# Kernel optimization log

Hardware: AMD Instinct MI355X
Metric: run time of the kernel (lower is better)

Reference implementation:

```python
import jax, jax.numpy as jnp
import numpy as np

B, D, V, S = 256, 784, 128, 2  # batch, dim, max_val, n_steps
ITER_PER_CYCLE = 10
STEP_SIZES = [0.5] + [0.1] * (ITER_PER_CYCLE - 1)   # sbc: [big_step] + [small_step]*...
BAL_CONSTS = [0.9] + [0.6] * (ITER_PER_CYCLE - 1)   # sbc: [big_bal] + [small_bal]*...
TEMP = 1.0


def setup_inputs() -> dict:
    key = jax.random.key(0)
    k1, k2, k3, k4, k5 = jax.random.split(key, 5)
    x = jax.random.randint(k1, (B, D), 0, V, dtype=jnp.int32)
    W = jax.random.normal(k2, (D, D), dtype=jnp.float32) * (1.0 / D)  # keep energies moderate
    b = jax.random.normal(k3, (D,), dtype=jnp.float32) * 0.1
    # Pre-sampled Gumbel noise for the categorical proposal (one slab per inner step)
    ug = jax.random.uniform(k4, (S, B, D, V), dtype=jnp.float32, minval=1e-6, maxval=1.0 - 1e-6)
    gumbel = -jnp.log(-jnp.log(ug))
    # Uniform draws for the MH accept/reject test
    u = jax.random.uniform(k5, (S, B), dtype=jnp.float32)
    k_iter = 0
    return {"x": x, "W": W, "b": b, "gumbel": gumbel, "u": u, "k_iter": k_iter}


def reference(x, W, b, gumbel, u, k_iter):
    step_size = STEP_SIZES[k_iter % ITER_PER_CYCLE]
    bal = BAL_CONSTS[k_iter % ITER_PER_CYCLE]
    Wsym = 0.5 * (W + W.T)

    def model(xf):                      # energy: [B]
        return 0.5 * jnp.einsum('bi,bi->b', xf, xf @ Wsym) + xf @ b

    def gradf(xf):                      # d(energy)/dx: [B, D]
        return xf @ Wsym + b

    disc = jnp.arange(V, dtype=jnp.float32)[None, None, :]  # [1,1,V]

    def calc_logits(xf, g):
        # term1 - term2 from _calc_logits, fused elementwise over [B, D, V]
        diff = disc - xf[:, :, None]
        return g[:, :, None] * diff * bal - diff * diff * (0.5 / step_size)

    def body(x_cur, inp):
        g_noise, ui = inp
        xf = x_cur.astype(jnp.float32)
        g = gradf(xf)
        logits = calc_logits(xf, g)                                  # [B,D,V]
        x_delta = jnp.argmax(logits + g_noise, axis=-1)              # categorical sample [B,D]
        logp = jax.nn.log_softmax(logits, axis=-1)
        lp_forward = jnp.take_along_axis(logp, x_delta[:, :, None], axis=-1)[..., 0].sum(axis=1)
        xdf = x_delta.astype(jnp.float32)
        gd = gradf(xdf) / TEMP
        logits_d = calc_logits(xdf, gd)
        logp_d = jax.nn.log_softmax(logits_d, axis=-1)
        lp_reverse = jnp.take_along_axis(logp_d, x_cur[:, :, None], axis=-1)[..., 0].sum(axis=1)
        la = model(xdf) - model(xf) + lp_reverse - lp_forward        # log accept ratio [B]
        acc = jnp.exp(la) > ui
        x_new = jnp.where(acc[:, None], x_delta, x_cur).astype(x_cur.dtype)
        return x_new, la

    x_out, las = jax.lax.scan(body, x, (gumbel, u))
    return x_out, las[-1]
```

## Files before the change

### kernel.cpp

```cpp
#include <hip/hip_runtime.h>

#define B_ 256
#define D_ 784
#define V_ 128
#define S_ 2
#define BD (B_ * D_)
#define KSPLIT 8
#define KC 98

__device__ __forceinline__ void get_params(const int* kiter, float& ss, float& bal) {
    int k = kiter[0] % 10;
    ss  = (k == 0) ? 0.5f : 0.1f;
    bal = (k == 0) ? 0.9f : 0.6f;
}

__device__ __forceinline__ double wave_red(double v) {
#pragma unroll
    for (int o = 32; o > 0; o >>= 1) v += __shfl_down(v, o, 64);
    return v;
}

__global__ __launch_bounds__(256) void symmetrize_k(
    const float* __restrict__ W, float* __restrict__ Wsym)
{
    __shared__ float tile[32][33];
    const int bx = blockIdx.x * 32, by = blockIdx.y * 32;
    const int tx = threadIdx.x & 31, ty4 = (threadIdx.x >> 5) * 4;
#pragma unroll
    for (int i = 0; i < 4; ++i) {
        int r = by + ty4 + i, c = bx + tx;
        tile[ty4 + i][tx] = (r < D_ && c < D_) ? W[r * D_ + c] : 0.f;
    }
    __syncthreads();
#pragma unroll
    for (int i = 0; i < 4; ++i) {
        int r = bx + ty4 + i, c = by + tx;
        if (r < D_ && c < D_)
            Wsym[r * D_ + c] = 0.5f * (W[r * D_ + c] + tile[tx][ty4 + i]);
    }
}

__global__ __launch_bounds__(256) void gemm_splitk(
    const int* __restrict__ Aint, const float* __restrict__ Wsym,
    float* __restrict__ Cp)
{
    const int bt = blockIdx.x, dt = blockIdx.y, kz = blockIdx.z;
    const int tid = threadIdx.x;
    const int k0 = kz * KC, kend = k0 + KC;

    __shared__ float As[64][20];
    __shared__ float Ws[16][68];

    const int tx = tid & 15, ty = tid >> 4;
    const int arow = tid >> 2, ac0 = (tid & 3) * 4;
    const int wrow = tid >> 4, wc0 = (tid & 15) * 4;
    const int wd0 = dt * 64 + wc0;

    float acc[4][4] = {};

    for (int kb = k0; kb < kend; kb += 16) {
#pragma unroll
        for (int c = 0; c < 4; ++c) {
            int k = kb + ac0 + c;
            As[arow][ac0 + c] = (k < kend) ? (float)Aint[(bt * 64 + arow) * D_ + k] : 0.f;
        }
        {
            int k = kb + wrow;
            float4 wv = (k < kend && wd0 < D_)
                ? *(const float4*)&Wsym[k * D_ + wd0]
                : make_float4(0.f, 0.f, 0.f, 0.f);
            *(float4*)&Ws[wrow][wc0] = wv;
        }
        __syncthreads();
#pragma unroll
        for (int kk = 0; kk < 16; kk += 4) {
            float va[4][4], vw[4][4];
#pragma unroll
            for (int i = 0; i < 4; ++i) {
                float4 t = *(const float4*)&As[ty * 4 + i][kk];
                va[i][0] = t.x; va[i][1] = t.y; va[i][2] = t.z; va[i][3] = t.w;
            }
#pragma unroll
            for (int m = 0; m < 4; ++m) {
                float4 t = *(const float4*)&Ws[kk + m][tx * 4];
                vw[m][0] = t.x; vw[m][1] = t.y; vw[m][2] = t.z; vw[m][3] = t.w;
            }
#pragma unroll
            for (int m = 0; m < 4; ++m)
#pragma unroll
                for (int i = 0; i < 4; ++i)
#pragma unroll
                    for (int j = 0; j < 4; ++j)
                        acc[i][j] = fmaf(va[i][m], vw[m][j], acc[i][j]);
        }
        __syncthreads();
    }

    const int d0 = dt * 64 + tx * 4;
    if (d0 < D_) {
#pragma unroll
        for (int i = 0; i < 4; ++i) {
            int bb = bt * 64 + ty * 4 + i;
            *(float4*)&Cp[(size_t)kz * BD + (size_t)bb * D_ + d0] =
                make_float4(acc[i][0], acc[i][1], acc[i][2], acc[i][3]);
        }
    }
}

__global__ __launch_bounds__(832) void forward_k(
    const int* __restrict__ xin, const float* __restrict__ gpart,
    const float* __restrict__ bvec, const float* __restrict__ gumbel,
    const int* __restrict__ kiter, int s,
    int* __restrict__ x_delta, double* __restrict__ lpf, double* __restrict__ Exf)
{
    const int b = blockIdx.x, tid = threadIdx.x;
    float ss, bal; get_params(kiter, ss, bal);
    const float c2 = 0.5f / ss;

    double lp_acc = 0.0, e_acc = 0.0;

    if (tid < D_) {
        const int d = tid, bd = b * D_ + d;
        const int xi = xin[bd];
        const float xfv = (float)xi;

        float gv = 0.f;
#pragma unroll
        for (int p = 0; p < KSPLIT; ++p) gv += gpart[(size_t)p * BD + bd];
        gv += bvec[d];

        const float a1 = bal * gv;
        const float v0 = xfv + a1 * ss;
        int vm = (int)rintf(v0); vm = min(127, max(0, vm));
        const float dmv = v0 - (float)vm;
        const float Reff = sqrtf(30.0f / c2 + dmv * dmv);
        int lo = max(0, (int)ceilf(v0 - Reff));
        int hi = min(127, (int)floorf(v0 + Reff));
        lo = min(lo, vm); hi = max(hi, vm);

        const float dvm = (float)vm - xfv;
        const float mL = dvm * fmaf(-c2, dvm, a1);

        const float4* __restrict__ gq =
            (const float4*)(gumbel + (((size_t)s * B_ + b) * D_ + d) * V_);
        const int q0 = lo >> 2, qh = hi >> 2;
        float4 quad[4];
#pragma unroll
        for (int j = 0; j < 4; ++j) quad[j] = gq[min(q0 + j, qh)];

        float best = -1e30f; int imax = vm;
        float sum0 = 0.f, sum1 = 0.f;
#pragma unroll
        for (int j = 0; j < 4; ++j) {
            const int qi = q0 + j;
            const bool qok = qi <= qh;
            const float qs[4] = {quad[j].x, quad[j].y, quad[j].z, quad[j].w};
#pragma unroll
            for (int c = 0; c < 4; ++c) {
                int v = 4 * qi + c;
                bool ok = qok && v >= lo && v <= hi;
                float dv = (float)v - xfv;
                float lg = dv * fmaf(-c2, dv, a1);
                float y = ok ? (lg + qs[c]) : -1e30f;
                if (y > best) { best = y; imax = v; }
                float e = expf(lg - mL);
                if (c & 1) sum1 += ok ? e : 0.f; else sum0 += ok ? e : 0.f;
            }
        }
        float lse = mL + logf(sum0 + sum1);
        float dvc = (float)imax - xfv;
        float lch = dvc * fmaf(-c2, dvc, a1);
        lp_acc = (double)(lch - lse);
        e_acc  = (double)xfv * ((double)gv + (double)bvec[d]);
        x_delta[bd] = imax;
    }

    __shared__ double wred[13];
    const int lane = tid & 63, wv = tid >> 6;
    double t = wave_red(lp_acc);
    if (lane == 0) wred[wv] = t;
    __syncthreads();
    if (tid == 0) { double sm = 0; for (int i = 0; i < 13; ++i) sm += wred[i]; lpf[b] = sm; }
    __syncthreads();
    t = wave_red(e_acc);
    if (lane == 0) wred[wv] = t;
    __syncthreads();
    if (tid == 0) { double sm = 0; for (int i = 0; i < 13; ++i) sm += wred[i]; Exf[b] = sm; }
}

__global__ __launch_bounds__(832) void reverse_k(
    const int* __restrict__ xin, int* __restrict__ x_cur,
    const int* __restrict__ x_delta,
    const float* __restrict__ gpart, const float* __restrict__ bvec,
    const float* __restrict__ u, const int* __restrict__ kiter,
    int s, int last, const double* __restrict__ lpf, const double* __restrict__ Exf,
    float* __restrict__ out)
{
    const int b = blockIdx.x, tid = threadIdx.x;
    float ss, bal; get_params(kiter, ss, bal);
    const float c2 = 0.5f / ss;

    double lp_acc = 0.0, e_acc = 0.0;

    if (tid < D_) {
        const int d = tid, bd = b * D_ + d;
        const int xi = xin[bd];
        const int xd = x_delta[bd];
        const float xdv = (float)xd;

        float gv = 0.f;
#pragma unroll
        for (int p = 0; p < KSPLIT; ++p) gv += gpart[(size_t)p * BD + bd];
        gv += bvec[d];

        const float a1 = bal * gv;
        const float v0 = xdv + a1 * ss;
        int vm = (int)rintf(v0); vm = min(127, max(0, vm));
        const float dmv = v0 - (float)vm;
        const float Reff = sqrtf(30.0f / c2 + dmv * dmv);
        int lo = max(0, (int)ceilf(v0 - Reff));
        int hi = min(127, (int)floorf(v0 + Reff));
        lo = min(lo, vm); hi = max(hi, vm);

        const float dvm = (float)vm - xdv;
        const float mL = dvm * fmaf(-c2, dvm, a1);
        float sum0 = 0.f, sum1 = 0.f;
#pragma unroll
        for (int j = 0; j < 16; ++j) {
            int v = lo + j;
            bool ok = v <= hi;
            float dv = (float)v - xdv;
            float lg = dv * fmaf(-c2, dv, a1);
            float e = expf(lg - mL);
            if (j & 1) sum1 += ok ? e : 0.f; else sum0 += ok ? e : 0.f;
        }
        float lse = mL + logf(sum0 + sum1);
        float dvc = (float)xi - xdv;
        float lch = dvc * fmaf(-c2, dvc, a1);
        lp_acc = (double)(lch - lse);
        e_acc  = (double)xdv * ((double)gv + (double)bvec[d]);
    }

    __shared__ double wred[13];
    __shared__ int accept_s;
    __shared__ float la_s;
    const int lane = tid & 63, wv = tid >> 6;

    double t = wave_red(lp_acc);
    if (lane == 0) wred[wv] = t;
    __syncthreads();
    double lpr = 0;
    if (tid == 0) { for (int i = 0; i < 13; ++i) lpr += wred[i]; }
    __syncthreads();
    t = wave_red(e_acc);
    if (lane == 0) wred[wv] = t;
    __syncthreads();
    if (tid == 0) {
        double exd = 0; for (int i = 0; i < 13; ++i) exd += wred[i];
        double la = 0.5 * (exd - Exf[b]) + lpr - lpf[b];
        accept_s = (exp(la) > (double)u[s * B_ + b]) ? 1 : 0;
        la_s = (float)la;
    }
    __syncthreads();

    const int acc = accept_s;
    if (tid < D_) {
        const int bd = b * D_ + tid;
        int xn = acc ? x_delta[bd] : xin[bd];
        x_cur[bd] = xn;
        if (last) out[bd] = (float)xn;
    }
    if (last && tid == 0) out[BD + b] = la_s;
}

extern "C" void kernel_launch(void* const* d_in, const int* in_sizes, int n_in,
                              void* d_out, int out_size, void* d_ws, size_t ws_size,
                              hipStream_t stream)
{
    const int*   x     = (const int*)d_in[0];
    const float* W     = (const float*)d_in[1];
    const float* bv    = (const float*)d_in[2];
    const float* gum   = (const float*)d_in[3];
    const float* u     = (const float*)d_in[4];
    const int*   kiter = (const int*)d_in[5];
    float* out = (float*)d_out;

    char* w = (char*)d_ws;
    size_t off = 0;
    auto carve = [&](size_t bytes) { void* p = w + off; off += (bytes + 511) & ~511ull; return p; };
    int*    x_cur   = (int*)   carve((size_t)BD * 4);
    int*    x_delta = (int*)   carve((size_t)BD * 4);
    float*  gpart   = (float*) carve((size_t)KSPLIT * BD * 4);
    double* lpf     = (double*)carve(B_ * 8);
    double* Exf     = (double*)carve(B_ * 8);
    float*  Wsym    = (float*) carve((size_t)D_ * D_ * 4);
    (void)ws_size; (void)in_sizes; (void)n_in; (void)out_size;

    symmetrize_k<<<dim3(25, 25), 256, 0, stream>>>(W, Wsym);

    for (int s = 0; s < S_; ++s) {
        const int* xin = (s == 0) ? x : x_cur;
        gemm_splitk<<<dim3(4, 13, KSPLIT), 256, 0, stream>>>(xin, Wsym, gpart);
        forward_k<<<B_, 832, 0, stream>>>(xin, gpart, bv, gum, kiter, s,
                                          x_delta, lpf, Exf);
        gemm_splitk<<<dim3(4, 13, KSPLIT), 256, 0, stream>>>(x_delta, Wsym, gpart);
        reverse_k<<<B_, 832, 0, stream>>>(xin, x_cur, x_delta, gpart, bv, u, kiter, s,
                                          (s == S_ - 1) ? 1 : 0, lpf, Exf, out);
    }
}
```

Measured before the change: 349.2 us.

## Fuse all stages into one cooperative persistent kernel with grid syncs

```diff
diff --git a/kernel.cpp b/kernel.cpp
--- a/kernel.cpp
+++ b/kernel.cpp
@@ -1,4 +1,7 @@
 #include <hip/hip_runtime.h>
+#include <hip/hip_cooperative_groups.h>
+
+namespace cg = cooperative_groups;
 
 #define B_ 256
 #define D_ 784
@@ -7,6 +10,10 @@
 #define BD (B_ * D_)
 #define KSPLIT 8
 #define KC 98
+#define NBLK 256
+#define NTHR 1024
+#define NJOBS (4 * 13 * KSPLIT)
+#define SUBSZ 2368
 
 __device__ __forceinline__ void get_params(const int* kiter, float& ss, float& bal) {
     int k = kiter[0] % 10;
@@ -20,51 +27,27 @@
     return v;
 }
 
-__global__ __launch_bounds__(256) void symmetrize_k(
-    const float* __restrict__ W, float* __restrict__ Wsym)
-{
-    __shared__ float tile[32][33];
-    const int bx = blockIdx.x * 32, by = blockIdx.y * 32;
-    const int tx = threadIdx.x & 31, ty4 = (threadIdx.x >> 5) * 4;
-#pragma unroll
-    for (int i = 0; i < 4; ++i) {
-        int r = by + ty4 + i, c = bx + tx;
-        tile[ty4 + i][tx] = (r < D_ && c < D_) ? W[r * D_ + c] : 0.f;
-    }
-    __syncthreads();
-#pragma unroll
-    for (int i = 0; i < 4; ++i) {
-        int r = bx + ty4 + i, c = by + tx;
-        if (r < D_ && c < D_)
-            Wsym[r * D_ + c] = 0.5f * (W[r * D_ + c] + tile[tx][ty4 + i]);
-    }
-}
-
-__global__ __launch_bounds__(256) void gemm_splitk(
-    const int* __restrict__ Aint, const float* __restrict__ Wsym,
-    float* __restrict__ Cp)
-{
-    const int bt = blockIdx.x, dt = blockIdx.y, kz = blockIdx.z;
-    const int tid = threadIdx.x;
+__device__ __forceinline__ void gemm_tile(
+    bool act, const int* __restrict__ A, const float* __restrict__ Wsym,
+    float* __restrict__ Cp, float* ldsbuf, int lt, int bt, int dt, int kz)
+{
+    float (*As)[20] = (float(*)[20])ldsbuf;
+    float (*Ws)[68] = (float(*)[68])(ldsbuf + 64 * 20);
     const int k0 = kz * KC, kend = k0 + KC;
-
-    __shared__ float As[64][20];
-    __shared__ float Ws[16][68];
-
-    const int tx = tid & 15, ty = tid >> 4;
-    const int arow = tid >> 2, ac0 = (tid & 3) * 4;
-    const int wrow = tid >> 4, wc0 = (tid & 15) * 4;
+    const int tx = lt & 15, ty = lt >> 4;
+    const int arow = lt >> 2, ac0 = (lt & 3) * 4;
+    const int wrow = lt >> 4, wc0 = (lt & 15) * 4;
     const int wd0 = dt * 64 + wc0;
 
     float acc[4][4] = {};
 
     for (int kb = k0; kb < kend; kb += 16) {
-#pragma unroll
-        for (int c = 0; c < 4; ++c) {
-            int k = kb + ac0 + c;
-            As[arow][ac0 + c] = (k < kend) ? (float)Aint[(bt * 64 + arow) * D_ + k] : 0.f;
-        }
-        {
+        if (act) {
+#pragma unroll
+            for (int c = 0; c < 4; ++c) {
+                int k = kb + ac0 + c;
+                As[arow][ac0 + c] = (k < kend) ? (float)A[(bt * 64 + arow) * D_ + k] : 0.f;
+            }
             int k = kb + wrow;
             float4 wv = (k < kend && wd0 < D_)
                 ? *(const float4*)&Wsym[k * D_ + wd0]
@@ -72,39 +55,292 @@
             *(float4*)&Ws[wrow][wc0] = wv;
         }
         __syncthreads();
-#pragma unroll
-        for (int kk = 0; kk < 16; kk += 4) {
-            float va[4][4], vw[4][4];
+        if (act) {
+#pragma unroll
+            for (int kk = 0; kk < 16; kk += 4) {
+                float va[4][4], vw[4][4];
+#pragma unroll
+                for (int i = 0; i < 4; ++i) {
+                    float4 t = *(const float4*)&As[ty * 4 + i][kk];
+                    va[i][0] = t.x; va[i][1] = t.y; va[i][2] = t.z; va[i][3] = t.w;
+                }
+#pragma unroll
+                for (int m = 0; m < 4; ++m) {
+                    float4 t = *(const float4*)&Ws[kk + m][tx * 4];
+                    vw[m][0] = t.x; vw[m][1] = t.y; vw[m][2] = t.z; vw[m][3] = t.w;
+                }
+#pragma unroll
+                for (int m = 0; m < 4; ++m)
+#pragma unroll
+                    for (int i = 0; i < 4; ++i)
+#pragma unroll
+                        for (int j = 0; j < 4; ++j)
+                            acc[i][j] = fmaf(va[i][m], vw[m][j], acc[i][j]);
+            }
+        }
+        __syncthreads();
+    }
+    if (act) {
+        const int d0 = dt * 64 + tx * 4;
+        if (d0 < D_) {
 #pragma unroll
             for (int i = 0; i < 4; ++i) {
-                float4 t = *(const float4*)&As[ty * 4 + i][kk];
-                va[i][0] = t.x; va[i][1] = t.y; va[i][2] = t.z; va[i][3] = t.w;
-            }
-#pragma unroll
-            for (int m = 0; m < 4; ++m) {
-                float4 t = *(const float4*)&Ws[kk + m][tx * 4];
-                vw[m][0] = t.x; vw[m][1] = t.y; vw[m][2] = t.z; vw[m][3] = t.w;
-            }
-#pragma unroll
-            for (int m = 0; m < 4; ++m)
-#pragma unroll
-                for (int i = 0; i < 4; ++i)
-#pragma unroll
-                    for (int j = 0; j < 4; ++j)
-                        acc[i][j] = fmaf(va[i][m], vw[m][j], acc[i][j]);
+                int bb = bt * 64 + ty * 4 + i;
+                *(float4*)&Cp[(size_t)kz * BD + (size_t)bb * D_ + d0] =
+                    make_float4(acc[i][0], acc[i][1], acc[i][2], acc[i][3]);
+            }
+        }
+    }
+}
+
+__global__ __launch_bounds__(NTHR, 4) void fused_k(
+    const int* __restrict__ x0, const float* __restrict__ W,
+    const float* __restrict__ bvec, const float* __restrict__ gumbel,
+    const float* __restrict__ u, const int* __restrict__ kiter,
+    float* __restrict__ out, int* __restrict__ x_cur,
+    int* __restrict__ x_delta, float* __restrict__ gpart,
+    float* __restrict__ Wsym)
+{
+    cg::grid_group grid = cg::this_grid();
+    const int bid = blockIdx.x, tid = threadIdx.x;
+    const int sub = tid >> 8, lt = tid & 255;
+
+    __shared__ __align__(16) float lds[4][SUBSZ];
+    __shared__ double wred[16];
+    __shared__ double lpf_s, exf_s;
+    __shared__ int accept_s;
+    __shared__ float la_s;
+
+    float ss, bal; get_params(kiter, ss, bal);
+    const float c2 = 0.5f / ss;
+
+    {
+        int t = bid + NBLK * sub;
+        bool act = t < 625;
+        int tt = act ? t : 0;
+        int ti = tt / 25, tj = tt % 25;
+        int bx = tj * 32, by = ti * 32;
+        float (*tile)[33] = (float(*)[33])lds[sub];
+        int ttx = lt & 31, tty4 = (lt >> 5) * 4;
+        if (act) {
+#pragma unroll
+            for (int i = 0; i < 4; ++i) {
+                int r = by + tty4 + i, c = bx + ttx;
+                tile[tty4 + i][ttx] = (r < D_ && c < D_) ? W[r * D_ + c] : 0.f;
+            }
         }
         __syncthreads();
-    }
-
-    const int d0 = dt * 64 + tx * 4;
-    if (d0 < D_) {
-#pragma unroll
-        for (int i = 0; i < 4; ++i) {
-            int bb = bt * 64 + ty * 4 + i;
-            *(float4*)&Cp[(size_t)kz * BD + (size_t)bb * D_ + d0] =
-                make_float4(acc[i][0], acc[i][1], acc[i][2], acc[i][3]);
-        }
-    }
+        if (act) {
+#pragma unroll
+            for (int i = 0; i < 4; ++i) {
+                int r = bx + tty4 + i, c = by + ttx;
+                if (r < D_ && c < D_)
+                    Wsym[r * D_ + c] = 0.5f * (W[r * D_ + c] + tile[ttx][tty4 + i]);
+            }
+        }
+    }
+    grid.sync();
+
+    for (int s = 0; s < S_; ++s) {
+        const int* xin = (s == 0) ? x0 : x_cur;
+
+        {
+            int job = bid + NBLK * sub;
+            bool act = job < NJOBS;
+            int j = act ? job : 0;
+            int kz = j % KSPLIT, td = j / KSPLIT;
+            int dt = td % 13, bt = td / 13;
+            gemm_tile(act, xin, Wsym, gpart, lds[sub], lt, bt, dt, kz);
+        }
+        grid.sync();
+
+        {
+            const int b = bid;
+            double lp_acc = 0.0, e_acc = 0.0;
+            if (tid < D_) {
+                const int d = tid, bd = b * D_ + d;
+                const int xi = xin[bd];
+                const float xfv = (float)xi;
+
+                float gv = 0.f;
+#pragma unroll
+                for (int p = 0; p < KSPLIT; ++p) gv += gpart[(size_t)p * BD + bd];
+                gv += bvec[d];
+
+                const float a1 = bal * gv;
+                const float v0 = xfv + a1 * ss;
+                int vm = (int)rintf(v0); vm = min(127, max(0, vm));
+                const float dmv = v0 - (float)vm;
+                const float Reff = sqrtf(30.0f / c2 + dmv * dmv);
+                int lo = max(0, (int)ceilf(v0 - Reff));
+                int hi = min(127, (int)floorf(v0 + Reff));
+                lo = min(lo, vm); hi = max(hi, vm);
+
+                const float dvm = (float)vm - xfv;
+                const float mL = dvm * fmaf(-c2, dvm, a1);
+
+                const float4* __restrict__ gq =
+                    (const float4*)(gumbel + (((size_t)s * B_ + b) * D_ + d) * V_);
+                const int q0 = lo >> 2, qh = hi >> 2;
+                float4 quad[4];
+#pragma unroll
+                for (int j = 0; j < 4; ++j) quad[j] = gq[min(q0 + j, qh)];
+
+                float best = -1e30f; int imax = vm;
+                float sum0 = 0.f, sum1 = 0.f;
+#pragma unroll
+                for (int j = 0; j < 4; ++j) {
+                    const int qi = q0 + j;
+                    const bool qok = qi <= qh;
+                    const float qs[4] = {quad[j].x, quad[j].y, quad[j].z, quad[j].w};
+#pragma unroll
+                    for (int c = 0; c < 4; ++c) {
+                        int v = 4 * qi + c;
+                        bool ok = qok && v >= lo && v <= hi;
+                        float dv = (float)v - xfv;
+                        float lg = dv * fmaf(-c2, dv, a1);
+                        float y = ok ? (lg + qs[c]) : -1e30f;
+                        if (y > best) { best = y; imax = v; }
+                        float e = expf(lg - mL);
+                        if (c & 1) sum1 += ok ? e : 0.f; else sum0 += ok ? e : 0.f;
+                    }
+                }
+                float lse = mL + logf(sum0 + sum1);
+                float dvc = (float)imax - xfv;
+                float lch = dvc * fmaf(-c2, dvc, a1);
+                lp_acc = (double)(lch - lse);
+                e_acc  = (double)xfv * ((double)gv + (double)bvec[d]);
+                x_delta[bd] = imax;
+            }
+            const int lane = tid & 63, wv = tid >> 6;
+            double t = wave_red(lp_acc);
+            if (lane == 0) wred[wv] = t;
+            __syncthreads();
+            if (tid == 0) { double sm = 0; for (int i = 0; i < 16; ++i) sm += wred[i]; lpf_s = sm; }
+            __syncthreads();
+            t = wave_red(e_acc);
+            if (lane == 0) wred[wv] = t;
+            __syncthreads();
+            if (tid == 0) { double sm = 0; for (int i = 0; i < 16; ++i) sm += wred[i]; exf_s = sm; }
+        }
+        grid.sync();
+
+        {
+            int job = bid + NBLK * sub;
+            bool act = job < NJOBS;
+            int j = act ? job : 0;
+            int kz = j % KSPLIT, td = j / KSPLIT;
+            int dt = td % 13, bt = td / 13;
+            gemm_tile(act, x_delta, Wsym, gpart, lds[sub], lt, bt, dt, kz);
+        }
+        grid.sync();
+
+        {
+            const int b = bid;
+            double lp_acc = 0.0, e_acc = 0.0;
+            if (tid < D_) {
+                const int d = tid, bd = b * D_ + d;
+                const int xi = xin[bd];
+                const int xd = x_delta[bd];
+                const float xdv = (float)xd;
+
+                float gv = 0.f;
+#pragma unroll
+                for (int p = 0; p < KSPLIT; ++p) gv += gpart[(size_t)p * BD + bd];
+                gv += bvec[d];
+
+                const float a1 = bal * gv;
+                const float v0 = xdv + a1 * ss;
+                int vm = (int)rintf(v0); vm = min(127, max(0, vm));
+                const float dmv = v0 - (float)vm;
+                const float Reff = sqrtf(30.0f / c2 + dmv * dmv);
+                int lo = max(0, (int)ceilf(v0 - Reff));
+                int hi = min(127, (int)floorf(v0 + Reff));
+                lo = min(lo, vm); hi = max(hi, vm);
+
+                const float dvm = (float)vm - xdv;
+                const float mL = dvm * fmaf(-c2, dvm, a1);
+                float sum0 = 0.f, sum1 = 0.f;
+#pragma unroll
+                for (int j = 0; j < 16; ++j) {
+                    int v = lo + j;
+                    bool ok = v <= hi;
+                    float dv = (float)v - xdv;
+                    float lg = dv * fmaf(-c2, dv, a1);
+                    float e = expf(lg - mL);
+                    if (j & 1) sum1 += ok ? e : 0.f; else sum0 += ok ? e : 0.f;
+                }
+                float lse = mL + logf(sum0 + sum1);
+                float dvc = (float)xi - xdv;
+                float lch = dvc * fmaf(-c2, dvc, a1);
+                lp_acc = (double)(lch - lse);
+                e_acc  = (double)xdv * ((double)gv + (double)bvec[d]);
+            }
+            const int lane = tid & 63, wv = tid >> 6;
+            double t = wave_red(lp_acc);
+            if (lane == 0) wred[wv] = t;
+            __syncthreads();
+            double lpr = 0;
+            if (tid == 0) { for (int i = 0; i < 16; ++i) lpr += wred[i]; }
+            __syncthreads();
+            t = wave_red(e_acc);
+            if (lane == 0) wred[wv] = t;
+            __syncthreads();
+            if (tid == 0) {
+                double exd = 0; for (int i = 0; i < 16; ++i) exd += wred[i];
+                double la = 0.5 * (exd - exf_s) + lpr - lpf_s;
+                accept_s = (exp(la) > (double)u[s * B_ + b]) ? 1 : 0;
+                la_s = (float)la;
+            }
+            __syncthreads();
+            const int acc = accept_s;
+            if (tid < D_) {
+                const int bd = b * D_ + tid;
+                int xn = acc ? x_delta[bd] : xin[bd];
+                x_cur[bd] = xn;
+                if (s == S_ - 1) out[bd] = (float)xn;
+            }
+            if (s == S_ - 1 && tid == 0) out[BD + b] = la_s;
+        }
+        if (s == 0) grid.sync();
+    }
+}
+
+__global__ __launch_bounds__(256) void symmetrize_k(
+    const float* __restrict__ W, float* __restrict__ Wsym)
+{
+    __shared__ float tile[32][33];
+    const int bx = blockIdx.x * 32, by = blockIdx.y * 32;
+    const int tx = threadIdx.x & 31, ty4 = (threadIdx.x >> 5) * 4;
+#pragma unroll
+    for (int i = 0; i < 4; ++i) {
+        int r = by + ty4 + i, c = bx + tx;
+        tile[ty4 + i][tx] = (r < D_ && c < D_) ? W[r * D_ + c] : 0.f;
+    }
+    __syncthreads();
+#pragma unroll
+    for (int i = 0; i < 4; ++i) {
+        int r = bx + ty4 + i, c = by + tx;
+        if (r < D_ && c < D_)
+            Wsym[r * D_ + c] = 0.5f * (W[r * D_ + c] + tile[tx][ty4 + i]);
+    }
+}
+
+__global__ __launch_bounds__(256) void gemm_splitk(
+    const int* __restrict__ Aint, const float* __restrict__ Wsym,
+    float* __restrict__ Cp)
+{
+    gemm_tile(true, Aint, Wsym, Cp,
+              nullptr, 0, 0, 0, 0);
+}
+
+__global__ __launch_bounds__(256) void gemm_splitk2(
+    const int* __restrict__ Aint, const float* __restrict__ Wsym,
+    float* __restrict__ Cp)
+{
+    __shared__ __align__(16) float buf[SUBSZ];
+    const int bt = blockIdx.x, dt = blockIdx.y, kz = blockIdx.z;
+    gemm_tile(true, Aint, Wsym, Cp, buf, threadIdx.x, bt, dt, kz);
 }
 
 __global__ __launch_bounds__(832) void forward_k(
@@ -116,19 +352,15 @@
     const int b = blockIdx.x, tid = threadIdx.x;
     float ss, bal; get_params(kiter, ss, bal);
     const float c2 = 0.5f / ss;
-
     double lp_acc = 0.0, e_acc = 0.0;
-
     if (tid < D_) {
         const int d = tid, bd = b * D_ + d;
         const int xi = xin[bd];
         const float xfv = (float)xi;
-
         float gv = 0.f;
 #pragma unroll
         for (int p = 0; p < KSPLIT; ++p) gv += gpart[(size_t)p * BD + bd];
         gv += bvec[d];
-
         const float a1 = bal * gv;
         const float v0 = xfv + a1 * ss;
         int vm = (int)rintf(v0); vm = min(127, max(0, vm));
@@ -137,17 +369,14 @@
         int lo = max(0, (int)ceilf(v0 - Reff));
         int hi = min(127, (int)floorf(v0 + Reff));
         lo = min(lo, vm); hi = max(hi, vm);
-
         const float dvm = (float)vm - xfv;
         const float mL = dvm * fmaf(-c2, dvm, a1);
-
         const float4* __restrict__ gq =
             (const float4*)(gumbel + (((size_t)s * B_ + b) * D_ + d) * V_);
         const int q0 = lo >> 2, qh = hi >> 2;
         float4 quad[4];
 #pragma unroll
         for (int j = 0; j < 4; ++j) quad[j] = gq[min(q0 + j, qh)];
-
         float best = -1e30f; int imax = vm;
         float sum0 = 0.f, sum1 = 0.f;
 #pragma unroll
@@ -174,7 +403,6 @@
         e_acc  = (double)xfv * ((double)gv + (double)bvec[d]);
         x_delta[bd] = imax;
     }
-
     __shared__ double wred[13];
     const int lane = tid & 63, wv = tid >> 6;
     double t = wave_red(lp_acc);
@@ -199,20 +427,16 @@
     const int b = blockIdx.x, tid = threadIdx.x;
     float ss, bal; get_params(kiter, ss, bal);
     const float c2 = 0.5f / ss;
-
     double lp_acc = 0.0, e_acc = 0.0;
-
     if (tid < D_) {
         const int d = tid, bd = b * D_ + d;
         const int xi = xin[bd];
         const int xd = x_delta[bd];
         const float xdv = (float)xd;
-
         float gv = 0.f;
 #pragma unroll
         for (int p = 0; p < KSPLIT; ++p) gv += gpart[(size_t)p * BD + bd];
         gv += bvec[d];
-
         const float a1 = bal * gv;
         const float v0 = xdv + a1 * ss;
         int vm = (int)rintf(v0); vm = min(127, max(0, vm));
@@ -221,7 +445,6 @@
         int lo = max(0, (int)ceilf(v0 - Reff));
         int hi = min(127, (int)floorf(v0 + Reff));
         lo = min(lo, vm); hi = max(hi, vm);
-
         const float dvm = (float)vm - xdv;
         const float mL = dvm * fmaf(-c2, dvm, a1);
         float sum0 = 0.f, sum1 = 0.f;
@@ -240,12 +463,10 @@
         lp_acc = (double)(lch - lse);
         e_acc  = (double)xdv * ((double)gv + (double)bvec[d]);
     }
-
     __shared__ double wred[13];
     __shared__ int accept_s;
     __shared__ float la_s;
     const int lane = tid & 63, wv = tid >> 6;
-
     double t = wave_red(lp_acc);
     if (lane == 0) wred[wv] = t;
     __syncthreads();
@@ -262,7 +483,6 @@
         la_s = (float)la;
     }
     __syncthreads();
-
     const int acc = accept_s;
     if (tid < D_) {
         const int bd = b * D_ + tid;
@@ -291,20 +511,27 @@
     int*    x_cur   = (int*)   carve((size_t)BD * 4);
     int*    x_delta = (int*)   carve((size_t)BD * 4);
     float*  gpart   = (float*) carve((size_t)KSPLIT * BD * 4);
+    float*  Wsym    = (float*) carve((size_t)D_ * D_ * 4);
     double* lpf     = (double*)carve(B_ * 8);
     double* Exf     = (double*)carve(B_ * 8);
-    float*  Wsym    = (float*) carve((size_t)D_ * D_ * 4);
     (void)ws_size; (void)in_sizes; (void)n_in; (void)out_size;
 
-    symmetrize_k<<<dim3(25, 25), 256, 0, stream>>>(W, Wsym);
-
-    for (int s = 0; s < S_; ++s) {
-        const int* xin = (s == 0) ? x : x_cur;
-        gemm_splitk<<<dim3(4, 13, KSPLIT), 256, 0, stream>>>(xin, Wsym, gpart);
-        forward_k<<<B_, 832, 0, stream>>>(xin, gpart, bv, gum, kiter, s,
-                                          x_delta, lpf, Exf);
-        gemm_splitk<<<dim3(4, 13, KSPLIT), 256, 0, stream>>>(x_delta, Wsym, gpart);
-        reverse_k<<<B_, 832, 0, stream>>>(xin, x_cur, x_delta, gpart, bv, u, kiter, s,
-                                          (s == S_ - 1) ? 1 : 0, lpf, Exf, out);
-    }
-}
+    void* args[] = { (void*)&x, (void*)&W, (void*)&bv, (void*)&gum, (void*)&u,
+                     (void*)&kiter, (void*)&out, (void*)&x_cur, (void*)&x_delta,
+                     (void*)&gpart, (void*)&Wsym };
+    hipError_t err = hipLaunchCooperativeKernel((const void*)fused_k,
+                                                dim3(NBLK), dim3(NTHR),
+                                                args, 0u, stream);
+    if (err != hipSuccess) {
+        symmetrize_k<<<dim3(25, 25), 256, 0, stream>>>(W, Wsym);
+        for (int s = 0; s < S_; ++s) {
+            const int* xin = (s == 0) ? x : x_cur;
+            gemm_splitk2<<<dim3(4, 13, KSPLIT), 256, 0, stream>>>(xin, Wsym, gpart);
+            forward_k<<<B_, 832, 0, stream>>>(xin, gpart, bv, gum, kiter, s,
+                                              x_delta, lpf, Exf);
+            gemm_splitk2<<<dim3(4, 13, KSPLIT), 256, 0, stream>>>(x_delta, Wsym, gpart);
+            reverse_k<<<B_, 832, 0, stream>>>(xin, x_cur, x_delta, gpart, bv, u, kiter, s,
+                                              (s == S_ - 1) ? 1 : 0, lpf, Exf, out);
+        }
+    }
+}
```

Result: slower. 629.3 us (+80.2%).

## Fuse split-K GEMM into forward and reverse kernels with row-blocked matvec

Applied to the files above, without the earlier changes.

```diff
diff --git a/kernel.cpp b/kernel.cpp
--- a/kernel.cpp
+++ b/kernel.cpp
@@ -5,8 +5,9 @@
 #define V_ 128
 #define S_ 2
 #define BD (B_ * D_)
-#define KSPLIT 8
-#define KC 98
+#define ROWS 4
+#define NBLKA 64
+#define NTHRA 512
 
 __device__ __forceinline__ void get_params(const int* kiter, float& ss, float& bal) {
     int k = kiter[0] % 10;
@@ -40,237 +41,243 @@
     }
 }
 
-__global__ __launch_bounds__(256) void gemm_splitk(
-    const int* __restrict__ Aint, const float* __restrict__ Wsym,
-    float* __restrict__ Cp)
-{
-    const int bt = blockIdx.x, dt = blockIdx.y, kz = blockIdx.z;
-    const int tid = threadIdx.x;
-    const int k0 = kz * KC, kend = k0 + KC;
-
-    __shared__ float As[64][20];
-    __shared__ float Ws[16][68];
-
-    const int tx = tid & 15, ty = tid >> 4;
-    const int arow = tid >> 2, ac0 = (tid & 3) * 4;
-    const int wrow = tid >> 4, wc0 = (tid & 15) * 4;
-    const int wd0 = dt * 64 + wc0;
-
-    float acc[4][4] = {};
-
-    for (int kb = k0; kb < kend; kb += 16) {
-#pragma unroll
-        for (int c = 0; c < 4; ++c) {
-            int k = kb + ac0 + c;
-            As[arow][ac0 + c] = (k < kend) ? (float)Aint[(bt * 64 + arow) * D_ + k] : 0.f;
-        }
-        {
-            int k = kb + wrow;
-            float4 wv = (k < kend && wd0 < D_)
-                ? *(const float4*)&Wsym[k * D_ + wd0]
-                : make_float4(0.f, 0.f, 0.f, 0.f);
-            *(float4*)&Ws[wrow][wc0] = wv;
-        }
-        __syncthreads();
-#pragma unroll
-        for (int kk = 0; kk < 16; kk += 4) {
-            float va[4][4], vw[4][4];
-#pragma unroll
-            for (int i = 0; i < 4; ++i) {
-                float4 t = *(const float4*)&As[ty * 4 + i][kk];
-                va[i][0] = t.x; va[i][1] = t.y; va[i][2] = t.z; va[i][3] = t.w;
-            }
-#pragma unroll
-            for (int m = 0; m < 4; ++m) {
-                float4 t = *(const float4*)&Ws[kk + m][tx * 4];
-                vw[m][0] = t.x; vw[m][1] = t.y; vw[m][2] = t.z; vw[m][3] = t.w;
-            }
-#pragma unroll
-            for (int m = 0; m < 4; ++m)
-#pragma unroll
-                for (int i = 0; i < 4; ++i)
-#pragma unroll
-                    for (int j = 0; j < 4; ++j)
-                        acc[i][j] = fmaf(va[i][m], vw[m][j], acc[i][j]);
-        }
-        __syncthreads();
-    }
-
-    const int d0 = dt * 64 + tx * 4;
-    if (d0 < D_) {
-#pragma unroll
-        for (int i = 0; i < 4; ++i) {
-            int bb = bt * 64 + ty * 4 + i;
-            *(float4*)&Cp[(size_t)kz * BD + (size_t)bb * D_ + d0] =
-                make_float4(acc[i][0], acc[i][1], acc[i][2], acc[i][3]);
-        }
-    }
-}
-
-__global__ __launch_bounds__(832) void forward_k(
-    const int* __restrict__ xin, const float* __restrict__ gpart,
+__global__ __launch_bounds__(NTHRA) void gemm_fwd_k(
+    const int* __restrict__ xin, const float* __restrict__ Wsym,
     const float* __restrict__ bvec, const float* __restrict__ gumbel,
     const int* __restrict__ kiter, int s,
     int* __restrict__ x_delta, double* __restrict__ lpf, double* __restrict__ Exf)
 {
-    const int b = blockIdx.x, tid = threadIdx.x;
+    const int bid = blockIdx.x, tid = threadIdx.x;
+    const int b0 = bid * ROWS;
     float ss, bal; get_params(kiter, ss, bal);
     const float c2 = 0.5f / ss;
 
-    double lp_acc = 0.0, e_acc = 0.0;
-
-    if (tid < D_) {
-        const int d = tid, bd = b * D_ + d;
-        const int xi = xin[bd];
-        const float xfv = (float)xi;
-
-        float gv = 0.f;
-#pragma unroll
-        for (int p = 0; p < KSPLIT; ++p) gv += gpart[(size_t)p * BD + bd];
-        gv += bvec[d];
-
-        const float a1 = bal * gv;
-        const float v0 = xfv + a1 * ss;
-        int vm = (int)rintf(v0); vm = min(127, max(0, vm));
-        const float dmv = v0 - (float)vm;
-        const float Reff = sqrtf(30.0f / c2 + dmv * dmv);
-        int lo = max(0, (int)ceilf(v0 - Reff));
-        int hi = min(127, (int)floorf(v0 + Reff));
-        lo = min(lo, vm); hi = max(hi, vm);
-
-        const float dvm = (float)vm - xfv;
-        const float mL = dvm * fmaf(-c2, dvm, a1);
-
-        const float4* __restrict__ gq =
-            (const float4*)(gumbel + (((size_t)s * B_ + b) * D_ + d) * V_);
-        const int q0 = lo >> 2, qh = hi >> 2;
-        float4 quad[4];
-#pragma unroll
-        for (int j = 0; j < 4; ++j) quad[j] = gq[min(q0 + j, qh)];
-
-        float best = -1e30f; int imax = vm;
-        float sum0 = 0.f, sum1 = 0.f;
-#pragma unroll
-        for (int j = 0; j < 4; ++j) {
-            const int qi = q0 + j;
-            const bool qok = qi <= qh;
-            const float qs[4] = {quad[j].x, quad[j].y, quad[j].z, quad[j].w};
-#pragma unroll
-            for (int c = 0; c < 4; ++c) {
-                int v = 4 * qi + c;
-                bool ok = qok && v >= lo && v <= hi;
-                float dv = (float)v - xfv;
-                float lg = dv * fmaf(-c2, dv, a1);
-                float y = ok ? (lg + qs[c]) : -1e30f;
-                if (y > best) { best = y; imax = v; }
-                float e = expf(lg - mL);
-                if (c & 1) sum1 += ok ? e : 0.f; else sum0 += ok ? e : 0.f;
+    __shared__ __align__(16) float af[D_][ROWS];
+    for (int idx = tid; idx < ROWS * D_; idx += NTHRA) {
+        int r = idx / D_, k = idx - r * D_;
+        af[k][r] = (float)xin[(b0 + r) * D_ + k];
+    }
+    __syncthreads();
+
+    const int d0 = tid;
+    const int d1 = tid + NTHRA;
+    const bool has1 = d1 < D_;
+
+    float acc[ROWS][2] = {};
+#pragma unroll 4
+    for (int k = 0; k < D_; ++k) {
+        float4 a4 = *(const float4*)&af[k][0];
+        float w0 = Wsym[k * D_ + d0];
+        float w1 = has1 ? Wsym[k * D_ + d1] : 0.f;
+        acc[0][0] = fmaf(a4.x, w0, acc[0][0]);
+        acc[1][0] = fmaf(a4.y, w0, acc[1][0]);
+        acc[2][0] = fmaf(a4.z, w0, acc[2][0]);
+        acc[3][0] = fmaf(a4.w, w0, acc[3][0]);
+        acc[0][1] = fmaf(a4.x, w1, acc[0][1]);
+        acc[1][1] = fmaf(a4.y, w1, acc[1][1]);
+        acc[2][1] = fmaf(a4.z, w1, acc[2][1]);
+        acc[3][1] = fmaf(a4.w, w1, acc[3][1]);
+    }
+
+    double lp_acc[ROWS] = {}, e_acc[ROWS] = {};
+#pragma unroll
+    for (int slot = 0; slot < 2; ++slot) {
+        const int d = slot ? d1 : d0;
+        if (d < D_) {
+            const float bvd = bvec[d];
+#pragma unroll
+            for (int r = 0; r < ROWS; ++r) {
+                const int b = b0 + r;
+                const float xfv = af[d][r];
+                const float gv = acc[r][slot] + bvd;
+
+                const float a1 = bal * gv;
+                const float v0 = xfv + a1 * ss;
+                int vm = (int)rintf(v0); vm = min(127, max(0, vm));
+                const float dmv = v0 - (float)vm;
+                const float Reff = sqrtf(30.0f / c2 + dmv * dmv);
+                int lo = max(0, (int)ceilf(v0 - Reff));
+                int hi = min(127, (int)floorf(v0 + Reff));
+                lo = min(lo, vm); hi = max(hi, vm);
+
+                const float dvm = (float)vm - xfv;
+                const float mL = dvm * fmaf(-c2, dvm, a1);
+
+                const float4* __restrict__ gq =
+                    (const float4*)(gumbel + (((size_t)s * B_ + b) * D_ + d) * V_);
+                const int q0 = lo >> 2, qh = hi >> 2;
+                float4 quad[4];
+#pragma unroll
+                for (int j = 0; j < 4; ++j) quad[j] = gq[min(q0 + j, qh)];
+
+                float best = -1e30f; int imax = vm;
+                float sum0 = 0.f, sum1 = 0.f;
+#pragma unroll
+                for (int j = 0; j < 4; ++j) {
+                    const int qi = q0 + j;
+                    const bool qok = qi <= qh;
+                    const float qs[4] = {quad[j].x, quad[j].y, quad[j].z, quad[j].w};
+#pragma unroll
+                    for (int c = 0; c < 4; ++c) {
+                        int v = 4 * qi + c;
+                        bool ok = qok && v >= lo && v <= hi;
+                        float dv = (float)v - xfv;
+                        float lg = dv * fmaf(-c2, dv, a1);
+                        float y = ok ? (lg + qs[c]) : -1e30f;
+                        if (y > best) { best = y; imax = v; }
+                        float e = expf(lg - mL);
+                        if (c & 1) sum1 += ok ? e : 0.f; else sum0 += ok ? e : 0.f;
+                    }
+                }
+                float lse = mL + logf(sum0 + sum1);
+                float dvc = (float)imax - xfv;
+                float lch = dvc * fmaf(-c2, dvc, a1);
+                lp_acc[r] += (double)(lch - lse);
+                e_acc[r]  += (double)xfv * ((double)gv + (double)bvd);
+                x_delta[b * D_ + d] = imax;
             }
         }
-        float lse = mL + logf(sum0 + sum1);
-        float dvc = (float)imax - xfv;
-        float lch = dvc * fmaf(-c2, dvc, a1);
-        lp_acc = (double)(lch - lse);
-        e_acc  = (double)xfv * ((double)gv + (double)bvec[d]);
-        x_delta[bd] = imax;
-    }
-
-    __shared__ double wred[13];
+    }
+
+    __shared__ double wred2[8][ROWS][2];
     const int lane = tid & 63, wv = tid >> 6;
-    double t = wave_red(lp_acc);
-    if (lane == 0) wred[wv] = t;
-    __syncthreads();
-    if (tid == 0) { double sm = 0; for (int i = 0; i < 13; ++i) sm += wred[i]; lpf[b] = sm; }
-    __syncthreads();
-    t = wave_red(e_acc);
-    if (lane == 0) wred[wv] = t;
-    __syncthreads();
-    if (tid == 0) { double sm = 0; for (int i = 0; i < 13; ++i) sm += wred[i]; Exf[b] = sm; }
-}
-
-__global__ __launch_bounds__(832) void reverse_k(
+#pragma unroll
+    for (int r = 0; r < ROWS; ++r) {
+        double t1 = wave_red(lp_acc[r]);
+        double t2 = wave_red(e_acc[r]);
+        if (lane == 0) { wred2[wv][r][0] = t1; wred2[wv][r][1] = t2; }
+    }
+    __syncthreads();
+    if (tid < ROWS) {
+        double sl = 0, se = 0;
+#pragma unroll
+        for (int i = 0; i < 8; ++i) { sl += wred2[i][tid][0]; se += wred2[i][tid][1]; }
+        lpf[b0 + tid] = sl;
+        Exf[b0 + tid] = se;
+    }
+}
+
+__global__ __launch_bounds__(NTHRA) void gemm_rev_k(
     const int* __restrict__ xin, int* __restrict__ x_cur,
-    const int* __restrict__ x_delta,
-    const float* __restrict__ gpart, const float* __restrict__ bvec,
-    const float* __restrict__ u, const int* __restrict__ kiter,
-    int s, int last, const double* __restrict__ lpf, const double* __restrict__ Exf,
+    const int* __restrict__ x_delta, const float* __restrict__ Wsym,
+    const float* __restrict__ bvec, const float* __restrict__ u,
+    const int* __restrict__ kiter, int s, int last,
+    const double* __restrict__ lpf, const double* __restrict__ Exf,
     float* __restrict__ out)
 {
-    const int b = blockIdx.x, tid = threadIdx.x;
+    const int bid = blockIdx.x, tid = threadIdx.x;
+    const int b0 = bid * ROWS;
     float ss, bal; get_params(kiter, ss, bal);
     const float c2 = 0.5f / ss;
 
-    double lp_acc = 0.0, e_acc = 0.0;
-
-    if (tid < D_) {
-        const int d = tid, bd = b * D_ + d;
-        const int xi = xin[bd];
-        const int xd = x_delta[bd];
-        const float xdv = (float)xd;
-
-        float gv = 0.f;
-#pragma unroll
-        for (int p = 0; p < KSPLIT; ++p) gv += gpart[(size_t)p * BD + bd];
-        gv += bvec[d];
-
-        const float a1 = bal * gv;
-        const float v0 = xdv + a1 * ss;
-        int vm = (int)rintf(v0); vm = min(127, max(0, vm));
-        const float dmv = v0 - (float)vm;
-        const float Reff = sqrtf(30.0f / c2 + dmv * dmv);
-        int lo = max(0, (int)ceilf(v0 - Reff));
-        int hi = min(127, (int)floorf(v0 + Reff));
-        lo = min(lo, vm); hi = max(hi, vm);
-
-        const float dvm = (float)vm - xdv;
-        const float mL = dvm * fmaf(-c2, dvm, a1);
-        float sum0 = 0.f, sum1 = 0.f;
-#pragma unroll
-        for (int j = 0; j < 16; ++j) {
-            int v = lo + j;
-            bool ok = v <= hi;
-            float dv = (float)v - xdv;
-            float lg = dv * fmaf(-c2, dv, a1);
-            float e = expf(lg - mL);
-            if (j & 1) sum1 += ok ? e : 0.f; else sum0 += ok ? e : 0.f;
+    __shared__ __align__(16) float af[D_][ROWS];
+    for (int idx = tid; idx < ROWS * D_; idx += NTHRA) {
+        int r = idx / D_, k = idx - r * D_;
+        af[k][r] = (float)x_delta[(b0 + r) * D_ + k];
+    }
+    __syncthreads();
+
+    const int d0 = tid;
+    const int d1 = tid + NTHRA;
+    const bool has1 = d1 < D_;
+
+    float acc[ROWS][2] = {};
+#pragma unroll 4
+    for (int k = 0; k < D_; ++k) {
+        float4 a4 = *(const float4*)&af[k][0];
+        float w0 = Wsym[k * D_ + d0];
+        float w1 = has1 ? Wsym[k * D_ + d1] : 0.f;
+        acc[0][0] = fmaf(a4.x, w0, acc[0][0]);
+        acc[1][0] = fmaf(a4.y, w0, acc[1][0]);
+        acc[2][0] = fmaf(a4.z, w0, acc[2][0]);
+        acc[3][0] = fmaf(a4.w, w0, acc[3][0]);
+        acc[0][1] = fmaf(a4.x, w1, acc[0][1]);
+        acc[1][1] = fmaf(a4.y, w1, acc[1][1]);
+        acc[2][1] = fmaf(a4.z, w1, acc[2][1]);
+        acc[3][1] = fmaf(a4.w, w1, acc[3][1]);
+    }
+
+    double lp_acc[ROWS] = {}, e_acc[ROWS] = {};
+    int xi_sav[ROWS][2], xd_sav[ROWS][2];
+#pragma unroll
+    for (int slot = 0; slot < 2; ++slot) {
+        const int d = slot ? d1 : d0;
+        if (d < D_) {
+            const float bvd = bvec[d];
+#pragma unroll
+            for (int r = 0; r < ROWS; ++r) {
+                const int bd = (b0 + r) * D_ + d;
+                const int xi = xin[bd];
+                const float xdv = af[d][r];
+                xi_sav[r][slot] = xi;
+                xd_sav[r][slot] = (int)xdv;
+                const float gv = acc[r][slot] + bvd;
+
+                const float a1 = bal * gv;
+                const float v0 = xdv + a1 * ss;
+                int vm = (int)rintf(v0); vm = min(127, max(0, vm));
+                const float dmv = v0 - (float)vm;
+                const float Reff = sqrtf(30.0f / c2 + dmv * dmv);
+                int lo = max(0, (int)ceilf(v0 - Reff));
+                int hi = min(127, (int)floorf(v0 + Reff));
+                lo = min(lo, vm); hi = max(hi, vm);
+
+                const float dvm = (float)vm - xdv;
+                const float mL = dvm * fmaf(-c2, dvm, a1);
+                float sum0 = 0.f, sum1 = 0.f;
+#pragma unroll
+                for (int j = 0; j < 16; ++j) {
+                    int v = lo + j;
+                    bool ok = v <= hi;
+                    float dv = (float)v - xdv;
+                    float lg = dv * fmaf(-c2, dv, a1);
+                    float e = expf(lg - mL);
+                    if (j & 1) sum1 += ok ? e : 0.f; else sum0 += ok ? e : 0.f;
+                }
+                float lse = mL + logf(sum0 + sum1);
+                float dvc = (float)xi - xdv;
+                float lch = dvc * fmaf(-c2, dvc, a1);
+                lp_acc[r] += (double)(lch - lse);
+                e_acc[r]  += (double)xdv * ((double)gv + (double)bvd);
+            }
         }
-        float lse = mL + logf(sum0 + sum1);
-        float dvc = (float)xi - xdv;
-        float lch = dvc * fmaf(-c2, dvc, a1);
-        lp_acc = (double)(lch - lse);
-        e_acc  = (double)xdv * ((double)gv + (double)bvec[d]);
-    }
-
-    __shared__ double wred[13];
-    __shared__ int accept_s;
-    __shared__ float la_s;
+    }
+
+    __shared__ double wred2[8][ROWS][2];
+    __shared__ int acc_fl[ROWS];
+    __shared__ float la_sh[ROWS];
     const int lane = tid & 63, wv = tid >> 6;
-
-    double t = wave_red(lp_acc);
-    if (lane == 0) wred[wv] = t;
-    __syncthreads();
-    double lpr = 0;
-    if (tid == 0) { for (int i = 0; i < 13; ++i) lpr += wred[i]; }
-    __syncthreads();
-    t = wave_red(e_acc);
-    if (lane == 0) wred[wv] = t;
-    __syncthreads();
-    if (tid == 0) {
-        double exd = 0; for (int i = 0; i < 13; ++i) exd += wred[i];
-        double la = 0.5 * (exd - Exf[b]) + lpr - lpf[b];
-        accept_s = (exp(la) > (double)u[s * B_ + b]) ? 1 : 0;
-        la_s = (float)la;
-    }
-    __syncthreads();
-
-    const int acc = accept_s;
-    if (tid < D_) {
-        const int bd = b * D_ + tid;
-        int xn = acc ? x_delta[bd] : xin[bd];
-        x_cur[bd] = xn;
-        if (last) out[bd] = (float)xn;
-    }
-    if (last && tid == 0) out[BD + b] = la_s;
+#pragma unroll
+    for (int r = 0; r < ROWS; ++r) {
+        double t1 = wave_red(lp_acc[r]);
+        double t2 = wave_red(e_acc[r]);
+        if (lane == 0) { wred2[wv][r][0] = t1; wred2[wv][r][1] = t2; }
+    }
+    __syncthreads();
+    if (tid < ROWS) {
+        double lpr = 0, exd = 0;
+#pragma unroll
+        for (int i = 0; i < 8; ++i) { lpr += wred2[i][tid][0]; exd += wred2[i][tid][1]; }
+        double la = 0.5 * (exd - Exf[b0 + tid]) + lpr - lpf[b0 + tid];
+        acc_fl[tid] = (exp(la) > (double)u[s * B_ + b0 + tid]) ? 1 : 0;
+        la_sh[tid] = (float)la;
+    }
+    __syncthreads();
+
+#pragma unroll
+    for (int slot = 0; slot < 2; ++slot) {
+        const int d = slot ? d1 : d0;
+        if (d < D_) {
+#pragma unroll
+            for (int r = 0; r < ROWS; ++r) {
+                const int bd = (b0 + r) * D_ + d;
+                int xn = acc_fl[r] ? xd_sav[r][slot] : xi_sav[r][slot];
+                x_cur[bd] = xn;
+                if (last) out[bd] = (float)xn;
+            }
+        }
+    }
+    if (last && tid < ROWS) out[BD + b0 + tid] = la_sh[tid];
 }
 
 extern "C" void kernel_launch(void* const* d_in, const int* in_sizes, int n_in,
@@ -290,21 +297,19 @@
     auto carve = [&](size_t bytes) { void* p = w + off; off += (bytes + 511) & ~511ull; return p; };
     int*    x_cur   = (int*)   carve((size_t)BD * 4);
     int*    x_delta = (int*)   carve((size_t)BD * 4);
-    float*  gpart   = (float*) carve((size_t)KSPLIT * BD * 4);
+    float*  Wsym    = (float*) carve((size_t)D_ * D_ * 4);
     double* lpf     = (double*)carve(B_ * 8);
     double* Exf     = (double*)carve(B_ * 8);
-    float*  Wsym    = (float*) carve((size_t)D_ * D_ * 4);
     (void)ws_size; (void)in_sizes; (void)n_in; (void)out_size;
 
     symmetrize_k<<<dim3(25, 25), 256, 0, stream>>>(W, Wsym);
 
     for (int s = 0; s < S_; ++s) {
         const int* xin = (s == 0) ? x : x_cur;
-        gemm_splitk<<<dim3(4, 13, KSPLIT), 256, 0, stream>>>(xin, Wsym, gpart);
-        forward_k<<<B_, 832, 0, stream>>>(xin, gpart, bv, gum, kiter, s,
-                                          x_delta, lpf, Exf);
-        gemm_splitk<<<dim3(4, 13, KSPLIT), 256, 0, stream>>>(x_delta, Wsym, gpart);
-        reverse_k<<<B_, 832, 0, stream>>>(xin, x_cur, x_delta, gpart, bv, u, kiter, s,
-                                          (s == S_ - 1) ? 1 : 0, lpf, Exf, out);
-    }
-}
+        gemm_fwd_k<<<NBLKA, NTHRA, 0, stream>>>(xin, Wsym, bv, gum, kiter, s,
+                                                x_delta, lpf, Exf);
+        gemm_rev_k<<<NBLKA, NTHRA, 0, stream>>>(xin, x_cur, x_delta, Wsym, bv, u,
+                                                kiter, s, (s == S_ - 1) ? 1 : 0,
+                                                lpf, Exf, out);
+    }
+}
```

Result: slower. 631.4 us (+80.8%).
